# Kernel tuning notes

Measured on AMD Instinct MI355X. Metric: run time of the kernel, lower is better.

Reference implementation:

```python
import jax, jax.numpy as jnp
import numpy as np

EPS = 1e-05
KARCHER_ITERS = 1  # Brooks-style BaryGeom: 1 Karcher-flow step from arithmetic mean


def _sym(X):
    return 0.5 * (X + jnp.swapaxes(X, -1, -2))


def _spd_fn(X, fn):
    # eigendecompose symmetric X, apply fn to eigenvalues, reconstruct
    w, V = jnp.linalg.eigh(_sym(X))
    return jnp.einsum('...ij,...j,...kj->...ik', V, fn(w), V)


def spd_pow(X, p):
    return _spd_fn(X, lambda w: w ** p)


def spd_log(X):
    return _spd_fn(X, jnp.log)


def spd_exp(X):
    return _spd_fn(X, jnp.exp)


def congr(X, G, mode):
    # CongrG: G^{-1/2} X G^{-1/2} ('neg') or G^{1/2} X G^{1/2} ('pos')
    Gh = spd_pow(G, -0.5 if mode == 'neg' else 0.5)
    return Gh @ X @ Gh


def karcher_mean(Xb):
    # Riemannian barycenter via Karcher flow, arithmetic-mean init (fn.BaryGeom)
    G = jnp.mean(Xb, axis=0)
    for _ in range(KARCHER_ITERS):
        Gs = spd_pow(G, 0.5)
        Gis = spd_pow(G, -0.5)
        GT = jnp.mean(spd_log(Gis @ Xb @ Gis), axis=0)  # tangent-space mean
        G = Gs @ spd_exp(GT) @ Gs
    return G


def setup_inputs() -> dict:
    key = jax.random.key(0)
    N, q, n = 1024, 32, 32
    kx, kr, kb = jax.random.split(key, 3)
    # batch of well-conditioned SPD matrices
    A = jax.random.normal(kx, (N, q, n, n), dtype=jnp.float32)
    X = A @ jnp.swapaxes(A, -1, -2) / n + 0.5 * jnp.eye(n, dtype=jnp.float32)
    # R: orthogonal (CanonicalStiefel) rotation parameter
    R = jnp.linalg.qr(jax.random.normal(kr, (n, n), dtype=jnp.float32))[0]
    # B: SPD bias parameter
    Ab = jax.random.normal(kb, (n, n), dtype=jnp.float32)
    B = Ab @ Ab.T / n + 0.5 * jnp.eye(n, dtype=jnp.float32)
    return {"X": X, "R": R, "B": B}


def reference(X, R, B):
    N, q, n, _ = X.shape
    Xb = X.reshape(N * q, n, n)
    # Karcher mean computed under no_grad in the original -> stop_gradient
    mean = jax.lax.stop_gradient(karcher_mean(Xb))
    # whiten (centre): mean^{-1/2} X mean^{-1/2}
    Xw = congr(Xb, mean, 'neg')
    # var = mean squared affine-invariant distance = mean ||log(Xw)||_F^2
    logs = spd_log(Xw)
    var = jnp.mean(jnp.sum(logs ** 2, axis=(-1, -2)))
    p = jnp.sqrt(1.0 / (var + EPS))
    # scale: PowerEig
    Xs = spd_pow(Xw, p)
    # rotate: bimap(X, R) = R X R^T
    Xr = R @ Xs @ R.T
    # bias (parallel shift): B^{1/2} X B^{1/2}
    Xo = congr(Xr, B, 'pos')
    return Xo.reshape(N, q, n, n)
```

## Files before the change

kernel.cpp:

```cpp
#include <hip/hip_runtime.h>
#include <math.h>

typedef float v2f __attribute__((ext_vector_type(2)));
typedef float v4f __attribute__((ext_vector_type(4)));

#define NMAT 32768
#define SW1 4
#define SW2 2
#define SW_SINGLE 10
#define SP 34

#define WS_G    0
#define WS_GS   1024
#define WS_GIS  2048
#define WS_GT   3072
#define WS_K    4096
#define WS_C    5120
#define WS_S1   6144
#define WS_S2   6145
#define WS_P    6146
#define WS_TOTAL 6400

__device__ __forceinline__ int swz(int r, int c) {
    return r * 32 + 2 * ((c >> 1) ^ (r & 15)) + (c & 1);
}

__device__ __forceinline__ void wave_fence() {
    asm volatile("s_waitcnt lgkmcnt(0)" ::: "memory");
}

template<int CTRL>
__device__ __forceinline__ float xsh(float x, int m) {
    if constexpr (CTRL != 0) {
        return __int_as_float(__builtin_amdgcn_update_dpp(
            __float_as_int(x), __float_as_int(x), CTRL, 0xF, 0xF, true));
    } else {
        return __shfl_xor(x, m, 64);
    }
}

template<int CTRL>
__device__ __forceinline__ void jac_round(v2f (&v)[16], int col, int m,
                                          float& dn, float& sc, float& rsc) {
    const float dnq = xsh<CTRL>(dn, m);
    const float dq  = xsh<CTRL>(sc, m);
    v2f o[16];
    #pragma unroll
    for (int j = 0; j < 16; ++j) {
        o[j].x = xsh<CTRL>(v[j].x, m);
        o[j].y = xsh<CTRL>(v[j].y, m);
    }
    v2f p0 = v[0] * o[0], p1 = v[1] * o[1], p2 = v[2] * o[2], p3 = v[3] * o[3];
    #pragma unroll
    for (int j = 4; j < 16; j += 4) {
        p0 += v[j] * o[j];     p1 += v[j + 1] * o[j + 1];
        p2 += v[j + 2] * o[j + 2]; p3 += v[j + 3] * o[j + 3];
    }
    v2f pt = (p0 + p1) + (p2 + p3);
    const float raw = pt.x + pt.y;
    const bool  isp = col < (col ^ m);
    const float apq = (sc * dq) * raw;
    const float b   = apq + apq;
    const float d   = isp ? (dnq - dn) : (dn - dnq);
    const float r2  = __builtin_fmaf(d, d, b * b);
    const float sr  = __builtin_amdgcn_sqrtf(r2);
    const float u   = fmaxf(fabsf(d) + sr, 1e-30f);
    const float t   = (d < 0.f ? -b : b) * __builtin_amdgcn_rcpf(u);
    const float s1  = __builtin_fmaf(t, t, 1.f);
    const float c   = __builtin_amdgcn_rsqf(s1);
    const float gam = t * (dq * rsc);
    const float gs  = isp ? -gam : gam;
    const v2f gs2 = {gs, gs};
    #pragma unroll
    for (int j = 0; j < 16; ++j) v[j] += gs2 * o[j];
    sc *= c; rsc *= c * s1;
    dn = __builtin_fmaf(isp ? -t : t, apq, dn);
}

__device__ __forceinline__ float jacobi_fg(v2f (&v)[16], int col, int sweeps) {
    float dn = 0.f;
    #pragma unroll 1
    for (int sweep = 0; sweep < sweeps; ++sweep) {
        {
            v2f n0 = v[0] * v[0], n1 = v[1] * v[1], n2 = v[2] * v[2], n3 = v[3] * v[3];
            #pragma unroll
            for (int j = 4; j < 16; j += 4) {
                n0 += v[j] * v[j];     n1 += v[j + 1] * v[j + 1];
                n2 += v[j + 2] * v[j + 2]; n3 += v[j + 3] * v[j + 3];
            }
            v2f nt = (n0 + n1) + (n2 + n3);
            dn = nt.x + nt.y;
        }
        float sc = 1.f, rsc = 1.f;
        jac_round<0xB1>(v, col, 1, dn, sc, rsc);
        jac_round<0x4E>(v, col, 2, dn, sc, rsc);
        jac_round<0x1B>(v, col, 3, dn, sc, rsc);
        #pragma unroll 1
        for (int m = 4; m < 32; ++m) jac_round<0>(v, col, m, dn, sc, rsc);
        const v2f s2 = {sc, sc};
        #pragma unroll
        for (int j = 0; j < 16; ++j) v[j] *= s2;
    }
    v2f n0 = v[0] * v[0], n1 = v[1] * v[1], n2 = v[2] * v[2], n3 = v[3] * v[3];
    #pragma unroll
    for (int j = 4; j < 16; j += 4) {
        n0 += v[j] * v[j];     n1 += v[j + 1] * v[j + 1];
        n2 += v[j + 2] * v[j + 2]; n3 += v[j + 3] * v[j + 3];
    }
    v2f nt = (n0 + n1) + (n2 + n3);
    return nt.x + nt.y;
}

__device__ __forceinline__ void put_col(float* L, const v2f (&w)[16], int col) {
    #pragma unroll
    for (int j = 0; j < 16; ++j) {
        L[(2 * j) * SP + col]     = w[j].x;
        L[(2 * j + 1) * SP + col] = w[j].y;
    }
}

__device__ __forceinline__ void colmm(const float* L, const v2f (&y)[16], v2f (&z)[16]) {
    #pragma unroll
    for (int i = 0; i < 32; ++i) {
        v2f acc = {0.f, 0.f};
        #pragma unroll
        for (int q = 0; q < 16; ++q) {
            v2f mm = *(const v2f*)&L[i * SP + 2 * q];
            acc += mm * y[q];
        }
        float zi = acc.x + acc.y;
        if (i & 1) z[i >> 1].y = zi; else z[i >> 1].x = zi;
    }
}

__device__ __forceinline__ void recon_col(const float* LW, float coef, int col,
                                          int base, v2f (&z)[16]) {
    float rv[32];
    #pragma unroll
    for (int k = 0; k < 32; ++k) rv[k] = LW[col * SP + k];
    v2f y[16];
    #pragma unroll
    for (int q = 0; q < 16; ++q) {
        y[q].x = __shfl(coef, base | (2 * q), 64)     * rv[2 * q];
        y[q].y = __shfl(coef, base | (2 * q + 1), 64) * rv[2 * q + 1];
    }
    colmm(LW, y, z);
}

__global__ __launch_bounds__(256) void k_mean(const float* __restrict__ X,
                                              float* __restrict__ ws) {
    const int t = threadIdx.x;
    const size_t base = (size_t)blockIdx.x * 64 * 1024;
    float4 a = {0.f, 0.f, 0.f, 0.f};
    for (int m = 0; m < 64; ++m) {
        float4 f = *(const float4*)&X[base + (size_t)m * 1024 + t * 4];
        a.x += f.x; a.y += f.y; a.z += f.z; a.w += f.w;
    }
    const float s = 1.0f / (float)NMAT;
    atomicAdd(ws + WS_G + 4 * t + 0, a.x * s);
    atomicAdd(ws + WS_G + 4 * t + 1, a.y * s);
    atomicAdd(ws + WS_G + 4 * t + 2, a.z * s);
    atomicAdd(ws + WS_G + 4 * t + 3, a.w * s);
}

__global__ __launch_bounds__(64) void k_small_prep(const float* __restrict__ R,
                                                   const float* __restrict__ B,
                                                   float* __restrict__ ws) {
    __shared__ float LW[32 * SP];
    const int lane = threadIdx.x;
    const int col  = lane & 31;
    const int base = lane & 32;
    if (blockIdx.x == 0) {
        v2f w[16];
        #pragma unroll
        for (int j = 0; j < 16; ++j) {
            w[j].x = ws[WS_G + (2 * j) * 32 + col];
            w[j].y = ws[WS_G + (2 * j + 1) * 32 + col];
        }
        const float dn = jacobi_fg(w, col, SW_SINGLE);
        put_col(LW, w, col);
        __syncthreads();
        const float lam = __builtin_amdgcn_sqrtf(dn);
        const float cs  = __builtin_amdgcn_sqrtf(lam) * __builtin_amdgcn_rcpf(dn);
        const float cis = __builtin_amdgcn_rsqf(lam)  * __builtin_amdgcn_rcpf(dn);
        v2f z[16];
        recon_col(LW, cs, col, base, z);
        #pragma unroll
        for (int j = 0; j < 16; ++j) {
            ws[WS_GS + (2 * j) * 32 + col]     = z[j].x;
            ws[WS_GS + (2 * j + 1) * 32 + col] = z[j].y;
        }
        recon_col(LW, cis, col, base, z);
        #pragma unroll
        for (int j = 0; j < 16; ++j) {
            ws[WS_GIS + (2 * j) * 32 + col]     = z[j].x;
            ws[WS_GIS + (2 * j + 1) * 32 + col] = z[j].y;
        }
    } else {
        v2f w[16];
        #pragma unroll
        for (int j = 0; j < 16; ++j) {
            w[j].x = B[(2 * j) * 32 + col];
            w[j].y = B[(2 * j + 1) * 32 + col];
        }
        const float dn = jacobi_fg(w, col, SW_SINGLE);
        put_col(LW, w, col);
        __syncthreads();
        const float lam = __builtin_amdgcn_sqrtf(dn);
        const float cbs = __builtin_amdgcn_sqrtf(lam) * __builtin_amdgcn_rcpf(dn);
        v2f bs[16];
        recon_col(LW, cbs, col, base, bs);
        __syncthreads();
        put_col(LW, bs, col);
        __syncthreads();
        v2f r[16];
        #pragma unroll
        for (int j = 0; j < 16; ++j) {
            r[j].x = R[(2 * j) * 32 + col];
            r[j].y = R[(2 * j + 1) * 32 + col];
        }
        v2f c[16];
        colmm(LW, r, c);
        #pragma unroll
        for (int j = 0; j < 16; ++j) {
            ws[WS_C + (2 * j) * 32 + col]     = c[j].x;
            ws[WS_C + (2 * j + 1) * 32 + col] = c[j].y;
        }
    }
}

__global__ __launch_bounds__(256, 6) void k_batch_log(const float* __restrict__ X,
                                                      float* __restrict__ w1out,
                                                      float* __restrict__ ws) {
    __shared__ float HL[1024];
    __shared__ float TW[4][1024];
    __shared__ float GB[4][2][32];
    __shared__ float ACC[1024];
    __shared__ float S1B, S2B;
    const int tid = threadIdx.x;
    if (tid == 0) { S1B = 0.f; S2B = 0.f; }
    for (int e = tid; e < 1024; e += 256) {
        int r = e >> 5, c = e & 31;
        HL[swz(r, c)] = ws[WS_GIS + e];
        ACC[e] = 0.f;
    }
    __syncthreads();

    const int lane = tid & 63;
    const int col  = lane & 31;
    const int half = lane >> 5;
    const int wv   = tid >> 6;
    const size_t gm = (size_t)blockIdx.x * 8 + wv * 2 + half;
    const float* Xm = X + gm * 1024;
    const int cm = col & 15, cbase = col * 32;
    float* tw = TW[wv];

    v2f h2[16];
    #pragma unroll
    for (int p = 0; p < 16; ++p) h2[p] = *(const v2f*)&HL[cbase + 2 * (p ^ cm)];

    v2f t2[16];
    #pragma unroll
    for (int i = 0; i < 32; ++i) {
        const float4* row = (const float4*)(Xm + i * 32);
        v2f acc = {0.f, 0.f};
        #pragma unroll
        for (int q = 0; q < 8; ++q) {
            float4 f = row[q];
            v2f lo = {f.x, f.y}, hi = {f.z, f.w};
            acc += lo * h2[2 * q] + hi * h2[2 * q + 1];
        }
        float ti = acc.x + acc.y;
        if (i & 1) t2[i >> 1].y = ti; else t2[i >> 1].x = ti;
    }
    v2f v[16];
    #pragma unroll
    for (int i = 0; i < 32; ++i) {
        v2f acc = {0.f, 0.f};
        const int twi = i & 15;
        #pragma unroll
        for (int q = 0; q < 8; ++q) {
            v4f f = *(const v4f*)&HL[i * 32 + 4 * q];
            v2f lo = {f.x, f.y}, hi = {f.z, f.w};
            acc += lo * t2[(2 * q) ^ twi] + hi * t2[(2 * q + 1) ^ twi];
        }
        float wi = acc.x + acc.y;
        if (i & 1) v[i >> 1].y = wi; else v[i >> 1].x = wi;
    }

    const float dn = jacobi_fg(v, col, SW1);

    float* outp = w1out + gm * 1024 + col;
    #pragma unroll
    for (int j = 0; j < 16; ++j) {
        outp[(2 * j) * 32]     = v[j].x;
        outp[(2 * j + 1) * 32] = v[j].y;
    }

    const float ls = 0.5f * logf(dn);
    const float g  = ls * __builtin_amdgcn_rcpf(dn) * (1.0f / (float)NMAT);
    {
        float s1 = ls, s2 = ls * ls;
        #pragma unroll
        for (int m = 32; m >= 1; m >>= 1) {
            s1 += __shfl_xor(s1, m, 64);
            s2 += __shfl_xor(s2, m, 64);
        }
        if (lane == 0) { atomicAdd(&S1B, s1); atomicAdd(&S2B, s2); }
    }

    float accR[16];
    #pragma unroll
    for (int i = 0; i < 16; ++i) accR[i] = 0.f;

    #pragma unroll 1
    for (int mm = 0; mm < 2; ++mm) {
        if (half == mm) {
            #pragma unroll
            for (int j = 0; j < 16; ++j) {
                tw[swz(2 * j, col)]     = v[j].x;
                tw[swz(2 * j + 1, col)] = v[j].y;
            }
            GB[wv][mm][col] = g;
        }
        wave_fence();
        v2f gr[16];
        #pragma unroll
        for (int p2 = 0; p2 < 16; ++p2) {
            v2f wr = *(const v2f*)&tw[cbase + 2 * (p2 ^ cm)];
            v2f gg = *(const v2f*)&GB[wv][mm][2 * p2];
            gr[p2] = gg * wr;
        }
        #pragma unroll
        for (int i = 0; i < 16; ++i) {
            const int r = half * 16 + i;
            const int rw = r & 15;
            v2f acc = {0.f, 0.f};
            #pragma unroll
            for (int q = 0; q < 8; ++q) {
                v4f f = *(const v4f*)&tw[r * 32 + 4 * q];
                v2f lo = {f.x, f.y}, hi = {f.z, f.w};
                acc += lo * gr[(2 * q) ^ rw] + hi * gr[(2 * q + 1) ^ rw];
            }
            accR[i] += acc.x + acc.y;
        }
        wave_fence();
    }
    #pragma unroll
    for (int i = 0; i < 16; ++i)
        atomicAdd(&ACC[(half * 16 + i) * 32 + col], accR[i]);
    __syncthreads();
    for (int e = tid; e < 1024; e += 256) atomicAdd(ws + WS_GT + e, ACC[e]);
    if (tid == 0) {
        atomicAdd(ws + WS_S1, S1B * (1.0f / (float)NMAT));
        atomicAdd(ws + WS_S2, S2B * (1.0f / (float)NMAT));
    }
}

__global__ __launch_bounds__(64) void k_karcher(float* __restrict__ ws) {
    __shared__ float LA[32 * SP];
    __shared__ float LB[32 * SP];
    const int lane = threadIdx.x;
    const int col  = lane & 31;
    const int base = lane & 32;

    for (int e = lane; e < 1024; e += 64)
        LB[(e >> 5) * SP + (e & 31)] = ws[WS_GS + e];
    v2f gsc[16];
    #pragma unroll
    for (int j = 0; j < 16; ++j) {
        gsc[j].x = ws[WS_GS + (2 * j) * 32 + col];
        gsc[j].y = ws[WS_GS + (2 * j + 1) * 32 + col];
    }
    v2f w[16];
    #pragma unroll
    for (int j = 0; j < 16; ++j) {
        w[j].x = ws[WS_GT + (2 * j) * 32 + col];
        w[j].y = ws[WS_GT + (2 * j + 1) * 32 + col];
    }
    v2f cn2 = {0.f, 0.f};
    #pragma unroll
    for (int j = 0; j < 16; ++j) cn2 += w[j] * w[j];
    float fro2 = cn2.x + cn2.y;
    #pragma unroll
    for (int m = 16; m >= 1; m >>= 1) fro2 += __shfl_xor(fro2, m, 64);
    const float shift = __builtin_amdgcn_sqrtf(fro2) + 0.01f;
    #pragma unroll
    for (int j = 0; j < 16; ++j) {
        w[j].x += (2 * j     == col) ? shift : 0.f;
        w[j].y += (2 * j + 1 == col) ? shift : 0.f;
    }
    const float dn = jacobi_fg(w, col, SW_SINGLE);
    put_col(LA, w, col);
    __syncthreads();
    const float lam = __builtin_amdgcn_sqrtf(dn) - shift;
    const float ce  = expf(lam) * __builtin_amdgcn_rcpf(dn);
    v2f ec[16];
    recon_col(LA, ce, col, base, ec);
    __syncthreads();
    put_col(LA, ec, col);
    __syncthreads();
    v2f u[16], gn[16];
    colmm(LA, gsc, u);
    colmm(LB, u, gn);
    const float dn2 = jacobi_fg(gn, col, SW_SINGLE);
    __syncthreads();
    put_col(LA, gn, col);
    __syncthreads();
    const float lam2 = __builtin_amdgcn_sqrtf(dn2);
    const float ch   = __builtin_amdgcn_rsqf(lam2) * __builtin_amdgcn_rcpf(dn2);
    v2f gh[16];
    recon_col(LA, ch, col, base, gh);
    __syncthreads();
    put_col(LA, gh, col);
    __syncthreads();
    v2f kc[16];
    colmm(LA, gsc, kc);
    #pragma unroll
    for (int j = 0; j < 16; ++j) {
        ws[WS_K + (2 * j) * 32 + col]     = kc[j].x;
        ws[WS_K + (2 * j + 1) * 32 + col] = kc[j].y;
    }
    if (lane == 0) {
        const float S1  = ws[WS_S1];
        const float S2  = ws[WS_S2];
        const float var = S2 - S1 * S1 * 0.03125f;
        ws[WS_P] = __builtin_amdgcn_rsqf(var + 1e-5f);
    }
}

__global__ __launch_bounds__(256, 6) void k_fused(float* __restrict__ out,
                                                  const float* __restrict__ ws) {
    __shared__ float KL[1024];
    __shared__ float CL[1024];
    __shared__ float TW[4][1024];
    const int tid = threadIdx.x;
    for (int e = tid; e < 1024; e += 256) {
        KL[e] = ws[WS_K + e];
        CL[e] = ws[WS_C + e];
    }
    __syncthreads();

    const int lane = tid & 63;
    const int col  = lane & 31;
    const int half = lane >> 5;
    const int wv   = tid >> 6;
    const size_t gmbase = (size_t)blockIdx.x * 8 + wv * 2;
    const size_t gm = gmbase + half;
    const int cm = col & 15, cbase = col * 32;
    float* tw = TW[wv];

    const float p = ws[WS_P];

    const float* wp = out + gm * 1024 + col;
    float w1[32];
    #pragma unroll
    for (int i = 0; i < 32; ++i) w1[i] = wp[i * 32];
    float nn = 0.f;
    #pragma unroll
    for (int i = 0; i < 32; ++i) nn = __builtin_fmaf(w1[i], w1[i], nn);
    const float s = __builtin_amdgcn_rsqf(__builtin_amdgcn_sqrtf(nn));
    v2f w1s[16];
    #pragma unroll
    for (int j = 0; j < 16; ++j) { w1s[j].x = w1[2 * j] * s; w1s[j].y = w1[2 * j + 1] * s; }

    v2f v[16];
    #pragma unroll
    for (int i = 0; i < 32; ++i) {
        v2f acc = {0.f, 0.f};
        #pragma unroll
        for (int q = 0; q < 8; ++q) {
            v4f f = *(const v4f*)&KL[i * 32 + 4 * q];
            v2f lo = {f.x, f.y}, hi = {f.z, f.w};
            acc += lo * w1s[2 * q] + hi * w1s[2 * q + 1];
        }
        float fi = acc.x + acc.y;
        if (i & 1) v[i >> 1].y = fi; else v[i >> 1].x = fi;
    }

    const float dn = jacobi_fg(v, col, SW2);
    const float dj = exp2f(log2f(dn) * 0.5f * (p - 1.0f));

    v2f yv[16];
    #pragma unroll
    for (int j = 0; j < 16; ++j) { yv[j].x = v[j].x * dj; yv[j].y = v[j].y * dj; }

    float y[32];
    #pragma unroll
    for (int i = 0; i < 32; ++i) {
        v2f acc = {0.f, 0.f};
        #pragma unroll
        for (int q = 0; q < 8; ++q) {
            v4f f = *(const v4f*)&CL[i * 32 + 4 * q];
            v2f lo = {f.x, f.y}, hi = {f.z, f.w};
            acc += lo * yv[2 * q] + hi * yv[2 * q + 1];
        }
        y[i] = acc.x + acc.y;
    }

    #pragma unroll 1
    for (int mm = 0; mm < 2; ++mm) {
        if (half == mm) {
            #pragma unroll
            for (int j = 0; j < 16; ++j) {
                tw[swz(2 * j, col)]     = y[2 * j];
                tw[swz(2 * j + 1, col)] = y[2 * j + 1];
            }
        }
        wave_fence();
        v2f yc[16];
        #pragma unroll
        for (int p2 = 0; p2 < 16; ++p2)
            yc[p2] = *(const v2f*)&tw[cbase + 2 * (p2 ^ cm)];
        const size_t gmo = gmbase + mm;
        #pragma unroll
        for (int i = 0; i < 16; ++i) {
            const int r = half * 16 + i;
            const int rw = r & 15;
            v2f acc = {0.f, 0.f};
            #pragma unroll
            for (int q = 0; q < 8; ++q) {
                v4f f = *(const v4f*)&tw[r * 32 + 4 * q];
                v2f lo = {f.x, f.y}, hi = {f.z, f.w};
                acc += lo * yc[(2 * q) ^ rw] + hi * yc[(2 * q + 1) ^ rw];
            }
            out[gmo * 1024 + r * 32 + col] = acc.x + acc.y;
        }
        wave_fence();
    }
}

extern "C" void kernel_launch(void* const* d_in, const int* in_sizes, int n_in,
                              void* d_out, int out_size, void* d_ws, size_t ws_size,
                              hipStream_t stream) {
    const float* X = (const float*)d_in[0];
    const float* R = (const float*)d_in[1];
    const float* B = (const float*)d_in[2];
    float* out = (float*)d_out;
    float* ws  = (float*)d_ws;

    hipMemsetAsync(d_ws, 0, WS_TOTAL * sizeof(float), stream);
    k_mean<<<NMAT / 64, 256, 0, stream>>>(X, ws);
    k_small_prep<<<2, 64, 0, stream>>>(R, B, ws);
    k_batch_log<<<NMAT / 8, 256, 0, stream>>>(X, out, ws);
    k_karcher<<<1, 64, 0, stream>>>(ws);
    k_fused<<<NMAT / 8, 256, 0, stream>>>(out, ws);
}
```

Baseline: 1.882 ms.

## Switch to two-column-per-lane block Jacobi with four matrices per wave

Reworks the one-sided Jacobi eigen-solver so each lane owns two columns and 16 lanes handle one matrix, which puts four matrices in each wave instead of two. Every lane-pair meeting now does four 2x2 rotations, so there are fewer cross-lane shuffles per rotation. Sweep counts rise from 4 to 5 and from 2 to 3 to keep convergence under the new rotation ordering. Register pressure grows, so the occupancy hint in launch_bounds drops from 6 to 3 and the grid is halved.

```diff
diff --git a/kernel.cpp b/kernel.cpp
--- a/kernel.cpp
+++ b/kernel.cpp
@@ -5,8 +5,8 @@
 typedef float v4f __attribute__((ext_vector_type(4)));
 
 #define NMAT 32768
-#define SW1 4
-#define SW2 2
+#define SW1 5
+#define SW2 3
 #define SW_SINGLE 10
 #define SP 34
 
@@ -24,10 +24,10 @@
 __device__ __forceinline__ int swz(int r, int c) {
     return r * 32 + 2 * ((c >> 1) ^ (r & 15)) + (c & 1);
 }
-
 __device__ __forceinline__ void wave_fence() {
     asm volatile("s_waitcnt lgkmcnt(0)" ::: "memory");
 }
+__device__ __forceinline__ v2f mk2(float a, float b) { v2f r; r.x = a; r.y = b; return r; }
 
 template<int CTRL>
 __device__ __forceinline__ float xsh(float x, int m) {
@@ -37,6 +37,101 @@
     } else {
         return __shfl_xor(x, m, 64);
     }
+}
+
+__device__ __forceinline__ float nrm16(const v2f (&v)[16]) {
+    v2f n0 = v[0] * v[0], n1 = v[1] * v[1], n2 = v[2] * v[2], n3 = v[3] * v[3];
+    #pragma unroll
+    for (int j = 4; j < 16; j += 4) {
+        n0 += v[j] * v[j];     n1 += v[j + 1] * v[j + 1];
+        n2 += v[j + 2] * v[j + 2]; n3 += v[j + 3] * v[j + 3];
+    }
+    v2f nt = (n0 + n1) + (n2 + n3);
+    return nt.x + nt.y;
+}
+
+__device__ __forceinline__ void rot2(v2f (&X)[16], v2f (&Y)[16],
+                                     float& dnX, float& dnY,
+                                     float& sX, float& rsX,
+                                     float& sY, float& rsY, bool low) {
+    v2f p0 = X[0] * Y[0], p1 = X[1] * Y[1], p2 = X[2] * Y[2], p3 = X[3] * Y[3];
+    #pragma unroll
+    for (int j = 4; j < 16; j += 4) {
+        p0 += X[j] * Y[j];         p1 += X[j + 1] * Y[j + 1];
+        p2 += X[j + 2] * Y[j + 2]; p3 += X[j + 3] * Y[j + 3];
+    }
+    v2f pt = (p0 + p1) + (p2 + p3);
+    const float raw = pt.x + pt.y;
+    const float apq = (sX * sY) * raw;
+    const float b   = apq + apq;
+    const float d   = dnY - dnX;
+    const float r2  = __builtin_fmaf(d, d, b * b);
+    const float sr  = __builtin_amdgcn_sqrtf(r2);
+    const float u   = fmaxf(fabsf(d) + sr, 1e-30f);
+    const bool  neg = (d < 0.f) || (d == 0.f && !low);
+    const float t   = (neg ? -b : b) * __builtin_amdgcn_rcpf(u);
+    const float s1f = __builtin_fmaf(t, t, 1.f);
+    const float c   = __builtin_amdgcn_rsqf(s1f);
+    const float rc  = c * s1f;
+    const float gX  = -t * (sY * rsX);
+    const float gY  =  t * (sX * rsY);
+    const v2f gX2 = {gX, gX}, gY2 = {gY, gY};
+    #pragma unroll
+    for (int j = 0; j < 16; ++j) {
+        const v2f yo = Y[j];
+        Y[j] = yo + gY2 * X[j];
+        X[j] = X[j] + gX2 * yo;
+    }
+    dnX = __builtin_fmaf(-t, apq, dnX);
+    dnY = __builtin_fmaf( t, apq, dnY);
+    sX *= c; rsX *= rc;
+    sY *= c; rsY *= rc;
+}
+
+template<int CTRL>
+__device__ __forceinline__ void meeting(v2f (&v0)[16], v2f (&v1)[16],
+                                        float& dn0, float& dn1,
+                                        float& s0, float& rs0,
+                                        float& s1_, float& rs1, int m, int g) {
+    const bool low = g < (g ^ m);
+    v2f c0[16], c1[16];
+    #pragma unroll
+    for (int j = 0; j < 16; ++j) {
+        c0[j].x = xsh<CTRL>(v0[j].x, m);
+        c0[j].y = xsh<CTRL>(v0[j].y, m);
+    }
+    float cdn0 = xsh<CTRL>(dn0, m), cs0 = xsh<CTRL>(s0, m), crs0 = xsh<CTRL>(rs0, m);
+    #pragma unroll
+    for (int j = 0; j < 16; ++j) {
+        c1[j].x = xsh<CTRL>(v1[j].x, m);
+        c1[j].y = xsh<CTRL>(v1[j].y, m);
+    }
+    float cdn1 = xsh<CTRL>(dn1, m), cs1 = xsh<CTRL>(s1_, m), crs1 = xsh<CTRL>(rs1, m);
+    rot2(v0, c0, dn0, cdn0, s0, rs0, cs0, crs0, low);
+    rot2(v1, c1, dn1, cdn1, s1_, rs1, cs1, crs1, low);
+    rot2(v0, c1, dn0, cdn1, s0, rs0, cs1, crs1, low);
+    rot2(v1, c0, dn1, cdn0, s1_, rs1, cs0, crs0, low);
+}
+
+__device__ __forceinline__ void jacobi_blk(v2f (&v0)[16], v2f (&v1)[16], int g,
+                                           int sweeps, float& odn0, float& odn1) {
+    #pragma unroll 1
+    for (int sw = 0; sw < sweeps; ++sw) {
+        float dn0 = nrm16(v0), dn1 = nrm16(v1);
+        float s0 = 1.f, rs0 = 1.f, s1_ = 1.f, rs1 = 1.f;
+        rot2(v0, v1, dn0, dn1, s0, rs0, s1_, rs1, true);
+        meeting<0xB1>(v0, v1, dn0, dn1, s0, rs0, s1_, rs1, 1, g);
+        meeting<0x4E>(v0, v1, dn0, dn1, s0, rs0, s1_, rs1, 2, g);
+        meeting<0x1B>(v0, v1, dn0, dn1, s0, rs0, s1_, rs1, 3, g);
+        #pragma unroll 1
+        for (int m = 4; m <= 15; ++m)
+            meeting<0>(v0, v1, dn0, dn1, s0, rs0, s1_, rs1, m, g);
+        const v2f f0 = {s0, s0}, f1 = {s1_, s1_};
+        #pragma unroll
+        for (int j = 0; j < 16; ++j) { v0[j] *= f0; v1[j] *= f1; }
+    }
+    odn0 = nrm16(v0);
+    odn1 = nrm16(v1);
 }
 
 template<int CTRL>
@@ -78,19 +173,9 @@
 }
 
 __device__ __forceinline__ float jacobi_fg(v2f (&v)[16], int col, int sweeps) {
-    float dn = 0.f;
     #pragma unroll 1
     for (int sweep = 0; sweep < sweeps; ++sweep) {
-        {
-            v2f n0 = v[0] * v[0], n1 = v[1] * v[1], n2 = v[2] * v[2], n3 = v[3] * v[3];
-            #pragma unroll
-            for (int j = 4; j < 16; j += 4) {
-                n0 += v[j] * v[j];     n1 += v[j + 1] * v[j + 1];
-                n2 += v[j + 2] * v[j + 2]; n3 += v[j + 3] * v[j + 3];
-            }
-            v2f nt = (n0 + n1) + (n2 + n3);
-            dn = nt.x + nt.y;
-        }
+        float dn = nrm16(v);
         float sc = 1.f, rsc = 1.f;
         jac_round<0xB1>(v, col, 1, dn, sc, rsc);
         jac_round<0x4E>(v, col, 2, dn, sc, rsc);
@@ -101,14 +186,7 @@
         #pragma unroll
         for (int j = 0; j < 16; ++j) v[j] *= s2;
     }
-    v2f n0 = v[0] * v[0], n1 = v[1] * v[1], n2 = v[2] * v[2], n3 = v[3] * v[3];
-    #pragma unroll
-    for (int j = 4; j < 16; j += 4) {
-        n0 += v[j] * v[j];     n1 += v[j + 1] * v[j + 1];
-        n2 += v[j + 2] * v[j + 2]; n3 += v[j + 3] * v[j + 3];
-    }
-    v2f nt = (n0 + n1) + (n2 + n3);
-    return nt.x + nt.y;
+    return nrm16(v);
 }
 
 __device__ __forceinline__ void put_col(float* L, const v2f (&w)[16], int col) {
@@ -229,12 +307,12 @@
     }
 }
 
-__global__ __launch_bounds__(256, 6) void k_batch_log(const float* __restrict__ X,
+__global__ __launch_bounds__(256, 3) void k_batch_log(const float* __restrict__ X,
                                                       float* __restrict__ w1out,
                                                       float* __restrict__ ws) {
     __shared__ float HL[1024];
     __shared__ float TW[4][1024];
-    __shared__ float GB[4][2][32];
+    __shared__ float GB[4][4][32];
     __shared__ float ACC[1024];
     __shared__ float S1B, S2B;
     const int tid = threadIdx.x;
@@ -247,88 +325,101 @@
     __syncthreads();
 
     const int lane = tid & 63;
-    const int col  = lane & 31;
-    const int half = lane >> 5;
     const int wv   = tid >> 6;
-    const size_t gm = (size_t)blockIdx.x * 8 + wv * 2 + half;
+    const int q    = lane >> 4;
+    const int g    = lane & 15;
+    const int c0   = 2 * g, c1 = 2 * g + 1;
+    const size_t gm = (size_t)blockIdx.x * 16 + wv * 4 + q;
     const float* Xm = X + gm * 1024;
-    const int cm = col & 15, cbase = col * 32;
     float* tw = TW[wv];
 
-    v2f h2[16];
-    #pragma unroll
-    for (int p = 0; p < 16; ++p) h2[p] = *(const v2f*)&HL[cbase + 2 * (p ^ cm)];
-
-    v2f t2[16];
+    v2f h0[16], h1[16];
+    const int e0 = c0 & 15, e1 = c1 & 15;
+    #pragma unroll
+    for (int p = 0; p < 16; ++p) {
+        h0[p] = *(const v2f*)&HL[c0 * 32 + 2 * (p ^ e0)];
+        h1[p] = *(const v2f*)&HL[c1 * 32 + 2 * (p ^ e1)];
+    }
+
+    v2f t0[16], t1[16];
     #pragma unroll
     for (int i = 0; i < 32; ++i) {
         const float4* row = (const float4*)(Xm + i * 32);
-        v2f acc = {0.f, 0.f};
-        #pragma unroll
-        for (int q = 0; q < 8; ++q) {
-            float4 f = row[q];
+        v2f a0 = {0.f, 0.f}, a1 = {0.f, 0.f};
+        #pragma unroll
+        for (int q8 = 0; q8 < 8; ++q8) {
+            float4 f = row[q8];
             v2f lo = {f.x, f.y}, hi = {f.z, f.w};
-            acc += lo * h2[2 * q] + hi * h2[2 * q + 1];
-        }
-        float ti = acc.x + acc.y;
-        if (i & 1) t2[i >> 1].y = ti; else t2[i >> 1].x = ti;
-    }
-    v2f v[16];
+            a0 += lo * h0[2 * q8] + hi * h0[2 * q8 + 1];
+            a1 += lo * h1[2 * q8] + hi * h1[2 * q8 + 1];
+        }
+        float u0 = a0.x + a0.y, u1 = a1.x + a1.y;
+        if (i & 1) { t0[i >> 1].y = u0; t1[i >> 1].y = u1; }
+        else       { t0[i >> 1].x = u0; t1[i >> 1].x = u1; }
+    }
+    v2f v0[16], v1[16];
     #pragma unroll
     for (int i = 0; i < 32; ++i) {
-        v2f acc = {0.f, 0.f};
         const int twi = i & 15;
-        #pragma unroll
-        for (int q = 0; q < 8; ++q) {
-            v4f f = *(const v4f*)&HL[i * 32 + 4 * q];
+        v2f a0 = {0.f, 0.f}, a1 = {0.f, 0.f};
+        #pragma unroll
+        for (int q8 = 0; q8 < 8; ++q8) {
+            v4f f = *(const v4f*)&HL[i * 32 + 4 * q8];
             v2f lo = {f.x, f.y}, hi = {f.z, f.w};
-            acc += lo * t2[(2 * q) ^ twi] + hi * t2[(2 * q + 1) ^ twi];
-        }
-        float wi = acc.x + acc.y;
-        if (i & 1) v[i >> 1].y = wi; else v[i >> 1].x = wi;
-    }
-
-    const float dn = jacobi_fg(v, col, SW1);
-
-    float* outp = w1out + gm * 1024 + col;
-    #pragma unroll
-    for (int j = 0; j < 16; ++j) {
-        outp[(2 * j) * 32]     = v[j].x;
-        outp[(2 * j + 1) * 32] = v[j].y;
-    }
-
-    const float ls = 0.5f * logf(dn);
-    const float g  = ls * __builtin_amdgcn_rcpf(dn) * (1.0f / (float)NMAT);
+            a0 += lo * t0[(2 * q8) ^ twi] + hi * t0[(2 * q8 + 1) ^ twi];
+            a1 += lo * t1[(2 * q8) ^ twi] + hi * t1[(2 * q8 + 1) ^ twi];
+        }
+        float u0 = a0.x + a0.y, u1 = a1.x + a1.y;
+        if (i & 1) { v0[i >> 1].y = u0; v1[i >> 1].y = u1; }
+        else       { v0[i >> 1].x = u0; v1[i >> 1].x = u1; }
+    }
+
+    float dn0, dn1;
+    jacobi_blk(v0, v1, g, SW1, dn0, dn1);
+
+    float* op = w1out + gm * 1024 + c0;
+    #pragma unroll
+    for (int j = 0; j < 16; ++j) {
+        *(v2f*)&op[(2 * j) * 32]     = mk2(v0[j].x, v1[j].x);
+        *(v2f*)&op[(2 * j + 1) * 32] = mk2(v0[j].y, v1[j].y);
+    }
+
+    const float ls0 = 0.5f * logf(dn0), ls1 = 0.5f * logf(dn1);
+    const float invN = 1.0f / (float)NMAT;
+    const float g0 = ls0 * __builtin_amdgcn_rcpf(dn0) * invN;
+    const float g1 = ls1 * __builtin_amdgcn_rcpf(dn1) * invN;
     {
-        float s1 = ls, s2 = ls * ls;
+        float s1v = ls0 + ls1, s2v = ls0 * ls0 + ls1 * ls1;
         #pragma unroll
         for (int m = 32; m >= 1; m >>= 1) {
-            s1 += __shfl_xor(s1, m, 64);
-            s2 += __shfl_xor(s2, m, 64);
-        }
-        if (lane == 0) { atomicAdd(&S1B, s1); atomicAdd(&S2B, s2); }
+            s1v += __shfl_xor(s1v, m, 64);
+            s2v += __shfl_xor(s2v, m, 64);
+        }
+        if (lane == 0) { atomicAdd(&S1B, s1v); atomicAdd(&S2B, s2v); }
     }
 
     float accR[16];
     #pragma unroll
     for (int i = 0; i < 16; ++i) accR[i] = 0.f;
+    const int cc = lane & 31, half = lane >> 5;
+    const int cm = cc & 15, cbase = cc * 32;
 
     #pragma unroll 1
-    for (int mm = 0; mm < 2; ++mm) {
-        if (half == mm) {
+    for (int s = 0; s < 4; ++s) {
+        if (q == s) {
             #pragma unroll
             for (int j = 0; j < 16; ++j) {
-                tw[swz(2 * j, col)]     = v[j].x;
-                tw[swz(2 * j + 1, col)] = v[j].y;
+                *(v2f*)&tw[(2 * j) * 32 + 2 * (g ^ ((2 * j) & 15))]         = mk2(v0[j].x, v1[j].x);
+                *(v2f*)&tw[(2 * j + 1) * 32 + 2 * (g ^ ((2 * j + 1) & 15))] = mk2(v0[j].y, v1[j].y);
             }
-            GB[wv][mm][col] = g;
+            *(v2f*)&GB[wv][s][c0] = mk2(g0, g1);
         }
         wave_fence();
         v2f gr[16];
         #pragma unroll
         for (int p2 = 0; p2 < 16; ++p2) {
             v2f wr = *(const v2f*)&tw[cbase + 2 * (p2 ^ cm)];
-            v2f gg = *(const v2f*)&GB[wv][mm][2 * p2];
+            v2f gg = *(const v2f*)&GB[wv][s][2 * p2];
             gr[p2] = gg * wr;
         }
         #pragma unroll
@@ -337,10 +428,10 @@
             const int rw = r & 15;
             v2f acc = {0.f, 0.f};
             #pragma unroll
-            for (int q = 0; q < 8; ++q) {
-                v4f f = *(const v4f*)&tw[r * 32 + 4 * q];
+            for (int q8 = 0; q8 < 8; ++q8) {
+                v4f f = *(const v4f*)&tw[r * 32 + 4 * q8];
                 v2f lo = {f.x, f.y}, hi = {f.z, f.w};
-                acc += lo * gr[(2 * q) ^ rw] + hi * gr[(2 * q + 1) ^ rw];
+                acc += lo * gr[(2 * q8) ^ rw] + hi * gr[(2 * q8 + 1) ^ rw];
             }
             accR[i] += acc.x + acc.y;
         }
@@ -348,12 +439,12 @@
     }
     #pragma unroll
     for (int i = 0; i < 16; ++i)
-        atomicAdd(&ACC[(half * 16 + i) * 32 + col], accR[i]);
+        atomicAdd(&ACC[(half * 16 + i) * 32 + cc], accR[i]);
     __syncthreads();
     for (int e = tid; e < 1024; e += 256) atomicAdd(ws + WS_GT + e, ACC[e]);
     if (tid == 0) {
-        atomicAdd(ws + WS_S1, S1B * (1.0f / (float)NMAT));
-        atomicAdd(ws + WS_S2, S2B * (1.0f / (float)NMAT));
+        atomicAdd(ws + WS_S1, S1B * invN);
+        atomicAdd(ws + WS_S2, S2B * invN);
     }
 }
 
@@ -429,7 +520,7 @@
     }
 }
 
-__global__ __launch_bounds__(256, 6) void k_fused(float* __restrict__ out,
+__global__ __launch_bounds__(256, 3) void k_fused(float* __restrict__ out,
                                                   const float* __restrict__ ws) {
     __shared__ float KL[1024];
     __shared__ float CL[1024];
@@ -442,69 +533,81 @@
     __syncthreads();
 
     const int lane = tid & 63;
-    const int col  = lane & 31;
-    const int half = lane >> 5;
     const int wv   = tid >> 6;
-    const size_t gmbase = (size_t)blockIdx.x * 8 + wv * 2;
-    const size_t gm = gmbase + half;
-    const int cm = col & 15, cbase = col * 32;
+    const int q    = lane >> 4;
+    const int g    = lane & 15;
+    const int c0   = 2 * g;
+    const size_t gmbase = (size_t)blockIdx.x * 16 + wv * 4;
+    const size_t gm = gmbase + q;
     float* tw = TW[wv];
-
     const float p = ws[WS_P];
 
-    const float* wp = out + gm * 1024 + col;
-    float w1[32];
-    #pragma unroll
-    for (int i = 0; i < 32; ++i) w1[i] = wp[i * 32];
-    float nn = 0.f;
-    #pragma unroll
-    for (int i = 0; i < 32; ++i) nn = __builtin_fmaf(w1[i], w1[i], nn);
-    const float s = __builtin_amdgcn_rsqf(__builtin_amdgcn_sqrtf(nn));
-    v2f w1s[16];
-    #pragma unroll
-    for (int j = 0; j < 16; ++j) { w1s[j].x = w1[2 * j] * s; w1s[j].y = w1[2 * j + 1] * s; }
-
-    v2f v[16];
+    const float* wp = out + gm * 1024 + c0;
+    v2f v0[16], v1[16];
+    #pragma unroll
+    for (int j = 0; j < 16; ++j) {
+        v2f la = *(const v2f*)&wp[(2 * j) * 32];
+        v2f lb = *(const v2f*)&wp[(2 * j + 1) * 32];
+        v0[j] = mk2(la.x, lb.x);
+        v1[j] = mk2(la.y, lb.y);
+    }
+    const float nn0 = nrm16(v0), nn1 = nrm16(v1);
+    const float sc0 = __builtin_amdgcn_rsqf(__builtin_amdgcn_sqrtf(nn0));
+    const float sc1 = __builtin_amdgcn_rsqf(__builtin_amdgcn_sqrtf(nn1));
+    v2f t0[16], t1[16];
+    const v2f sv0 = {sc0, sc0}, sv1 = {sc1, sc1};
+    #pragma unroll
+    for (int j = 0; j < 16; ++j) { t0[j] = v0[j] * sv0; t1[j] = v1[j] * sv1; }
+
     #pragma unroll
     for (int i = 0; i < 32; ++i) {
-        v2f acc = {0.f, 0.f};
-        #pragma unroll
-        for (int q = 0; q < 8; ++q) {
-            v4f f = *(const v4f*)&KL[i * 32 + 4 * q];
+        v2f a0 = {0.f, 0.f}, a1 = {0.f, 0.f};
+        #pragma unroll
+        for (int q8 = 0; q8 < 8; ++q8) {
+            v4f f = *(const v4f*)&KL[i * 32 + 4 * q8];
             v2f lo = {f.x, f.y}, hi = {f.z, f.w};
-            acc += lo * w1s[2 * q] + hi * w1s[2 * q + 1];
-        }
-        float fi = acc.x + acc.y;
-        if (i & 1) v[i >> 1].y = fi; else v[i >> 1].x = fi;
-    }
-
-    const float dn = jacobi_fg(v, col, SW2);
-    const float dj = exp2f(log2f(dn) * 0.5f * (p - 1.0f));
-
-    v2f yv[16];
-    #pragma unroll
-    for (int j = 0; j < 16; ++j) { yv[j].x = v[j].x * dj; yv[j].y = v[j].y * dj; }
-
-    float y[32];
+            a0 += lo * t0[2 * q8] + hi * t0[2 * q8 + 1];
+            a1 += lo * t1[2 * q8] + hi * t1[2 * q8 + 1];
+        }
+        float u0 = a0.x + a0.y, u1 = a1.x + a1.y;
+        if (i & 1) { v0[i >> 1].y = u0; v1[i >> 1].y = u1; }
+        else       { v0[i >> 1].x = u0; v1[i >> 1].x = u1; }
+    }
+
+    float dn0, dn1;
+    jacobi_blk(v0, v1, g, SW2, dn0, dn1);
+
+    const float dj0 = exp2f(log2f(dn0) * 0.5f * (p - 1.0f));
+    const float dj1 = exp2f(log2f(dn1) * 0.5f * (p - 1.0f));
+    const v2f dv0 = {dj0, dj0}, dv1 = {dj1, dj1};
+    #pragma unroll
+    for (int j = 0; j < 16; ++j) { t0[j] = v0[j] * dv0; t1[j] = v1[j] * dv1; }
+
+    v2f y0[16], y1[16];
     #pragma unroll
     for (int i = 0; i < 32; ++i) {
-        v2f acc = {0.f, 0.f};
-        #pragma unroll
-        for (int q = 0; q < 8; ++q) {
-            v4f f = *(const v4f*)&CL[i * 32 + 4 * q];
+        v2f a0 = {0.f, 0.f}, a1 = {0.f, 0.f};
+        #pragma unroll
+        for (int q8 = 0; q8 < 8; ++q8) {
+            v4f f = *(const v4f*)&CL[i * 32 + 4 * q8];
             v2f lo = {f.x, f.y}, hi = {f.z, f.w};
-            acc += lo * yv[2 * q] + hi * yv[2 * q + 1];
-        }
-        y[i] = acc.x + acc.y;
-    }
-
+            a0 += lo * t0[2 * q8] + hi * t0[2 * q8 + 1];
+            a1 += lo * t1[2 * q8] + hi * t1[2 * q8 + 1];
+        }
+        float u0 = a0.x + a0.y, u1 = a1.x + a1.y;
+        if (i & 1) { y0[i >> 1].y = u0; y1[i >> 1].y = u1; }
+        else       { y0[i >> 1].x = u0; y1[i >> 1].x = u1; }
+    }
+
+    const int cc = lane & 31, half = lane >> 5;
+    const int cm = cc & 15, cbase = cc * 32;
     #pragma unroll 1
-    for (int mm = 0; mm < 2; ++mm) {
-        if (half == mm) {
+    for (int s = 0; s < 4; ++s) {
+        if (q == s) {
             #pragma unroll
             for (int j = 0; j < 16; ++j) {
-                tw[swz(2 * j, col)]     = y[2 * j];
-                tw[swz(2 * j + 1, col)] = y[2 * j + 1];
+                *(v2f*)&tw[(2 * j) * 32 + 2 * (g ^ ((2 * j) & 15))]         = mk2(y0[j].x, y1[j].x);
+                *(v2f*)&tw[(2 * j + 1) * 32 + 2 * (g ^ ((2 * j + 1) & 15))] = mk2(y0[j].y, y1[j].y);
             }
         }
         wave_fence();
@@ -512,19 +615,19 @@
         #pragma unroll
         for (int p2 = 0; p2 < 16; ++p2)
             yc[p2] = *(const v2f*)&tw[cbase + 2 * (p2 ^ cm)];
-        const size_t gmo = gmbase + mm;
+        const size_t gmo = gmbase + s;
         #pragma unroll
         for (int i = 0; i < 16; ++i) {
             const int r = half * 16 + i;
             const int rw = r & 15;
             v2f acc = {0.f, 0.f};
             #pragma unroll
-            for (int q = 0; q < 8; ++q) {
-                v4f f = *(const v4f*)&tw[r * 32 + 4 * q];
+            for (int q8 = 0; q8 < 8; ++q8) {
+                v4f f = *(const v4f*)&tw[r * 32 + 4 * q8];
                 v2f lo = {f.x, f.y}, hi = {f.z, f.w};
-                acc += lo * yc[(2 * q) ^ rw] + hi * yc[(2 * q + 1) ^ rw];
+                acc += lo * yc[(2 * q8) ^ rw] + hi * yc[(2 * q8 + 1) ^ rw];
             }
-            out[gmo * 1024 + r * 32 + col] = acc.x + acc.y;
+            out[gmo * 1024 + r * 32 + cc] = acc.x + acc.y;
         }
         wave_fence();
     }
@@ -542,7 +645,7 @@
     hipMemsetAsync(d_ws, 0, WS_TOTAL * sizeof(float), stream);
     k_mean<<<NMAT / 64, 256, 0, stream>>>(X, ws);
     k_small_prep<<<2, 64, 0, stream>>>(R, B, ws);
-    k_batch_log<<<NMAT / 8, 256, 0, stream>>>(X, out, ws);
+    k_batch_log<<<NMAT / 16, 256, 0, stream>>>(X, out, ws);
     k_karcher<<<1, 64, 0, stream>>>(ws);
-    k_fused<<<NMAT / 8, 256, 0, stream>>>(out, ws);
-}
+    k_fused<<<NMAT / 16, 256, 0, stream>>>(out, ws);
+}
```

After: 4.743 ms. 2.52x slower.
